# Optimization experiments

Hardware: AMD Instinct MI355X
Metric: run time of the kernel (lower is better)

Reference implementation:

```python
import jax, jax.numpy as jnp
import numpy as np

B, S, I, H = 32, 512, 1024, 1024


def _rnn_pass(x, W_ih, W_hh, b_ih, b_hh):
    # x: [B,S,I]; vanilla tanh RNN, h0 = 0. Precompute input projection once.
    xp = jnp.einsum('bsi,hi->bsh', x, W_ih) + b_ih + b_hh  # [B,S,H]
    h0 = jnp.zeros((x.shape[0], W_hh.shape[0]), dtype=x.dtype)

    def step(h, xp_t):
        h_new = jnp.tanh(xp_t + h @ W_hh.T)
        return h_new, h_new

    _, outs = jax.lax.scan(step, h0, jnp.swapaxes(xp, 0, 1))  # [S,B,H]
    return jnp.swapaxes(outs, 0, 1)  # [B,S,H]


def setup_inputs() -> dict:
    key = jax.random.key(0)
    ks = jax.random.split(key, 9)
    scale_i = 1.0 / np.sqrt(I)
    scale_h = 1.0 / np.sqrt(H)
    return {
        'x': jax.random.normal(ks[0], (B, S, I), dtype=jnp.float32),
        'W_ih_f': jax.random.normal(ks[1], (H, I), dtype=jnp.float32) * scale_i,
        'W_hh_f': jax.random.normal(ks[2], (H, H), dtype=jnp.float32) * scale_h,
        'b_ih_f': jax.random.normal(ks[3], (H,), dtype=jnp.float32) * scale_h,
        'b_hh_f': jax.random.normal(ks[4], (H,), dtype=jnp.float32) * scale_h,
        'W_ih_b': jax.random.normal(ks[5], (H, I), dtype=jnp.float32) * scale_i,
        'W_hh_b': jax.random.normal(ks[6], (H, H), dtype=jnp.float32) * scale_h,
        'b_ih_b': jax.random.normal(ks[7], (H,), dtype=jnp.float32) * scale_h,
        'b_hh_b': jax.random.normal(ks[8], (H,), dtype=jnp.float32) * scale_h,
    }


def reference(x, W_ih_f, W_hh_f, b_ih_f, b_hh_f, W_ih_b, W_hh_b, b_ih_b, b_hh_b):
    fwd = _rnn_pass(x, W_ih_f, W_hh_f, b_ih_f, b_hh_f)              # [B,S,H]
    bwd = _rnn_pass(x[:, ::-1, :], W_ih_b, W_hh_b, b_ih_b, b_hh_b)  # reversed seq
    bwd = bwd[:, ::-1, :]                                           # flip back
    return jnp.concatenate([fwd, bwd], axis=-1)  # [B,S,2H]
```

## Files before the change

kernel.cpp:

```cpp
#include <hip/hip_runtime.h>

typedef _Float16 half8  __attribute__((ext_vector_type(8)));
typedef _Float16 half4v __attribute__((ext_vector_type(4)));
typedef float    floatx4 __attribute__((ext_vector_type(4)));
typedef unsigned long long u64;

#define B_ 32
#define S_ 512
#define I_ 1024
#define H_ 1024
#define M_TOT (B_ * S_)

__global__ void cvt_f32_f16(const float* __restrict__ src, _Float16* __restrict__ dst, long n) {
  long i = ((long)blockIdx.x * blockDim.x + threadIdx.x) * 4;
  const long stride = (long)gridDim.x * blockDim.x * 4;
  for (; i < n; i += stride) {
    floatx4 v = *(const floatx4*)(src + i);
    half4v h = {(_Float16)v[0], (_Float16)v[1], (_Float16)v[2], (_Float16)v[3]};
    *(half4v*)(dst + i) = h;
  }
}

__global__ void bias_sum_kernel(const float* __restrict__ bihf, const float* __restrict__ bhhf,
                                const float* __restrict__ bihb, const float* __restrict__ bhhb,
                                float* __restrict__ bias, unsigned int* __restrict__ counter) {
  int i = blockIdx.x * blockDim.x + threadIdx.x;
  if (i == 0) {
    __hip_atomic_store(counter,      0u, __ATOMIC_RELAXED, __HIP_MEMORY_SCOPE_AGENT);
    __hip_atomic_store(counter + 32, 0u, __ATOMIC_RELAXED, __HIP_MEMORY_SCOPE_AGENT);
  }
  if (i < H_) {
    bias[i]      = bihf[i] + bhhf[i];
    bias[H_ + i] = bihb[i] + bhhb[i];
  }
}

__global__ void __launch_bounds__(256) gemm_xp_kernel(
    const _Float16* __restrict__ A,
    const _Float16* __restrict__ W,
    const float*    __restrict__ bias,
    float*          __restrict__ out)
{
  __shared__ _Float16 alds[128 * 32];
  __shared__ _Float16 blds[128 * 32];

  const int dir = blockIdx.z;
  const int m0  = blockIdx.y * 128;
  const int n0  = blockIdx.x * 128;
  const int tid  = threadIdx.x;
  const int lane = tid & 63;
  const int wv   = tid >> 6;
  const int wm   = wv >> 1, wn = wv & 1;
  const int lrow = lane & 15;
  const int lkg  = lane >> 4;

  const _Float16* Wd = W + (long)dir * H_ * I_;

  floatx4 acc[4][4] = {};

  const int srow = tid >> 1;
  const int sseg = tid & 1;

  for (int kt = 0; kt < 32; ++kt) {
    __syncthreads();
    {
      const _Float16* srcA = A  + (long)(m0 + srow) * I_ + kt * 32 + sseg * 16;
      const _Float16* srcB = Wd + (long)(n0 + srow) * I_ + kt * 32 + sseg * 16;
      half8 a0 = *(const half8*)(srcA);
      half8 a1 = *(const half8*)(srcA + 8);
      half8 b0 = *(const half8*)(srcB);
      half8 b1 = *(const half8*)(srcB + 8);
      const int sw = (srow & 7) << 4;
      const int base = srow * 64 + sseg * 32;
      *(half8*)((char*)alds + ((base     ) ^ sw)) = a0;
      *(half8*)((char*)alds + ((base + 16) ^ sw)) = a1;
      *(half8*)((char*)blds + ((base     ) ^ sw)) = b0;
      *(half8*)((char*)blds + ((base + 16) ^ sw)) = b1;
    }
    __syncthreads();

    half8 af[4], bf[4];
#pragma unroll
    for (int mt = 0; mt < 4; ++mt) {
      int r = wm * 64 + mt * 16 + lrow;
      int byte = (r * 64 + lkg * 16) ^ ((r & 7) << 4);
      af[mt] = *(const half8*)((const char*)alds + byte);
    }
#pragma unroll
    for (int ntt = 0; ntt < 4; ++ntt) {
      int r = wn * 64 + ntt * 16 + lrow;
      int byte = (r * 64 + lkg * 16) ^ ((r & 7) << 4);
      bf[ntt] = *(const half8*)((const char*)blds + byte);
    }
#pragma unroll
    for (int mt = 0; mt < 4; ++mt)
#pragma unroll
      for (int ntt = 0; ntt < 4; ++ntt)
        acc[mt][ntt] = __builtin_amdgcn_mfma_f32_16x16x32_f16(af[mt], bf[ntt], acc[mt][ntt], 0, 0, 0);
  }

#pragma unroll
  for (int mt = 0; mt < 4; ++mt) {
    int mrow = m0 + wm * 64 + mt * 16 + lkg * 4;
#pragma unroll
    for (int ntt = 0; ntt < 4; ++ntt) {
      int n = n0 + wn * 64 + ntt * 16 + lrow;
      float bv = bias[dir * H_ + n];
#pragma unroll
      for (int v = 0; v < 4; ++v) {
        out[(long)(mrow + v) * (2 * H_) + dir * H_ + n] = acc[mt][ntt][v] + bv;
      }
    }
  }
}

__global__ void __launch_bounds__(256, 1) scan_kernel(
    const float* __restrict__ Whh_f,
    const float* __restrict__ Whh_b,
    float*       __restrict__ out,
    _Float16*    __restrict__ hbuf,
    unsigned int* __restrict__ counter)
{
  __shared__ _Float16 wlds[32 * 1024];
  __shared__ floatx4  redlds[4 * 64];

  const int w     = blockIdx.x;
  const int dir   = w >> 5;
  const int rows0 = (w & 31) * 32;
  const float* Whh = dir ? Whh_b : Whh_f;
  unsigned int* ctr = counter + dir * 32;
  const int tid = threadIdx.x;

  for (int idx = tid; idx < 32 * 128; idx += 256) {
    const int r  = idx >> 7;
    const int kg = idx & 127;
    const float* src = Whh + (long)(rows0 + r) * H_ + kg * 8;
    floatx4 v0 = *(const floatx4*)(src);
    floatx4 v1 = *(const floatx4*)(src + 4);
    half8 h = {(_Float16)v0[0], (_Float16)v0[1], (_Float16)v0[2], (_Float16)v0[3],
               (_Float16)v1[0], (_Float16)v1[1], (_Float16)v1[2], (_Float16)v1[3]};
    const int byte = (r * 2048 + kg * 16) ^ ((r & 7) << 4);
    *(half8*)((char*)wlds + byte) = h;
  }

  {
    const int b  = tid >> 3;
    const int rg = tid & 7;
    u64* p = (u64*)(hbuf + ((long)(0 * 2 + dir) * B_ + b) * H_ + rows0 + rg * 4);
    __hip_atomic_store(p, (u64)0, __ATOMIC_RELAXED, __HIP_MEMORY_SCOPE_AGENT);
  }

  const int lane = tid & 63;
  const int wv   = tid >> 6;
  const int nt   = wv & 1;
  const int kh   = wv >> 1;
  const int lrow = lane & 15;
  const int lkg  = lane >> 4;
  const int b_idx = nt * 16 + lrow;
  const int kbase = kh * 512;
  const int r0    = rows0 + kh * 16 + lkg * 4;
  const int asw   = (lrow & 7) << 4;
  const int abase0 = lrow * 2048 + kbase * 2;
  const int abase1 = (16 + lrow) * 2048 + kbase * 2;

  unsigned int bar = 32;

  asm volatile("s_waitcnt vmcnt(0)" ::: "memory");
  __syncthreads();
  if (tid == 0) {
    __hip_atomic_fetch_add(ctr, 1u, __ATOMIC_RELAXED, __HIP_MEMORY_SCOPE_AGENT);
    while (__hip_atomic_load(ctr, __ATOMIC_RELAXED, __HIP_MEMORY_SCOPE_AGENT) < bar) {
      __builtin_amdgcn_s_sleep(1);
    }
  }
  __syncthreads();

  long o_next;
  {
    const int sidx = dir ? (S_ - 1) : 0;
    o_next = ((long)b_idx * S_ + sidx) * (2 * H_) + dir * H_ + r0;
  }
  floatx4 xp_next = *(const floatx4*)(out + o_next);

  for (int t = 0; t < S_; ++t) {
    const int p = t & 1;

    const _Float16* hp = hbuf + ((long)(p * 2 + dir) * B_ + b_idx) * H_ + kbase + lkg * 8;
    half8 hr[16];
#pragma unroll
    for (int kt = 0; kt < 16; ++kt) {
      asm volatile("global_load_dwordx4 %0, %1, off offset:%2 sc1"
                   : "=v"(hr[kt]) : "v"(hp), "i"(kt * 64) : "memory");
    }
    asm volatile("s_waitcnt vmcnt(0)" ::: "memory");
    __builtin_amdgcn_sched_barrier(0);

    floatx4 acc0 = {}, acc1 = {};
#pragma unroll
    for (int kt = 0; kt < 16; ++kt) {
      const int koff = kt * 64 + lkg * 16;
      half8 a0 = *(const half8*)((const char*)wlds + ((abase0 + koff) ^ asw));
      half8 a1 = *(const half8*)((const char*)wlds + ((abase1 + koff) ^ asw));
      acc0 = __builtin_amdgcn_mfma_f32_16x16x32_f16(a0, hr[kt], acc0, 0, 0, 0);
      acc1 = __builtin_amdgcn_mfma_f32_16x16x32_f16(a1, hr[kt], acc1, 0, 0, 0);
    }

    redlds[((1 - kh) * 2 + nt) * 64 + lane] = kh ? acc0 : acc1;
    __syncthreads();
    floatx4 tot = (kh ? acc1 : acc0) + redlds[(kh * 2 + nt) * 64 + lane];

    const long o = o_next;
    const floatx4 xpv = xp_next;
    if (t + 1 < S_) {
      const int sidx1 = dir ? (S_ - 2 - t) : (t + 1);
      o_next = ((long)b_idx * S_ + sidx1) * (2 * H_) + dir * H_ + r0;
      xp_next = *(const floatx4*)(out + o_next);
    }

    floatx4 hv;
#pragma unroll
    for (int v = 0; v < 4; ++v) {
      float z = tot[v] + xpv[v];
      hv[v] = 1.f - 2.f / (__expf(2.f * z) + 1.f);
    }
    *(floatx4*)(out + o) = hv;

    if (t + 1 < S_) {
      union { half4v h; u64 u; } hh;
      hh.h = half4v{(_Float16)hv[0], (_Float16)hv[1], (_Float16)hv[2], (_Float16)hv[3]};
      u64* dst = (u64*)(hbuf + ((long)((1 - p) * 2 + dir) * B_ + b_idx) * H_ + r0);
      __hip_atomic_store(dst, hh.u, __ATOMIC_RELAXED, __HIP_MEMORY_SCOPE_AGENT);
    } else {
      break;
    }

    bar += 32;
    asm volatile("s_waitcnt vmcnt(0)" ::: "memory");
    __syncthreads();
    if (tid == 0) {
      __hip_atomic_fetch_add(ctr, 1u, __ATOMIC_RELAXED, __HIP_MEMORY_SCOPE_AGENT);
      while (__hip_atomic_load(ctr, __ATOMIC_RELAXED, __HIP_MEMORY_SCOPE_AGENT) < bar) {
        __builtin_amdgcn_s_sleep(1);
      }
    }
    __syncthreads();
  }
}

extern "C" void kernel_launch(void* const* d_in, const int* in_sizes, int n_in,
                              void* d_out, int out_size, void* d_ws, size_t ws_size,
                              hipStream_t stream) {
  const float* x    = (const float*)d_in[0];
  const float* Wihf = (const float*)d_in[1];
  const float* Whhf = (const float*)d_in[2];
  const float* bihf = (const float*)d_in[3];
  const float* bhhf = (const float*)d_in[4];
  const float* Wihb = (const float*)d_in[5];
  const float* Whhb = (const float*)d_in[6];
  const float* bihb = (const float*)d_in[7];
  const float* bhhb = (const float*)d_in[8];
  float* out = (float*)d_out;

  char* ws = (char*)d_ws;
  _Float16*     x16  = (_Float16*)ws;
  _Float16*     w16  = (_Float16*)(ws + 33554432u);
  float*        bias = (float*)   (ws + 33554432u + 4194304u);
  _Float16*     hbuf = (_Float16*)(ws + 37756928u);
  unsigned int* counter = (unsigned int*)(ws + 38019072u);

  cvt_f32_f16<<<4096, 256, 0, stream>>>(x, x16, (long)M_TOT * I_);
  cvt_f32_f16<<<1024, 256, 0, stream>>>(Wihf, w16, (long)H_ * I_);
  cvt_f32_f16<<<1024, 256, 0, stream>>>(Wihb, w16 + (long)H_ * I_, (long)H_ * I_);
  bias_sum_kernel<<<4, 256, 0, stream>>>(bihf, bhhf, bihb, bhhb, bias, counter);

  dim3 g(H_ / 128, M_TOT / 128, 2);
  gemm_xp_kernel<<<g, 256, 0, stream>>>(x16, w16, bias, out);

  void* args[] = {(void*)&Whhf, (void*)&Whhb, (void*)&out, (void*)&hbuf, (void*)&counter};
  (void)hipLaunchCooperativeKernel((void*)scan_kernel, dim3(64), dim3(256),
                                   args, 0, stream);
}
```

Before: 2.446 ms.

## Interleave forward and backward RNN steps per block with split barrier counters

Each of the 64 blocks now owns 16 hidden rows of both directions rather than 32 rows of one direction, and it alternates forward and backward step computation. Each direction gets its own arrival counter. A block signals one direction, then computes the other direction before waiting on the first, so the latency of the grid-wide barrier is meant to overlap with useful MFMA work. In exchange, each block does two smaller matvecs per step with more __syncthreads. The per-step work per block also becomes more serialized, and the extra global counter traffic adds risk.

```diff
diff --git a/kernel.cpp b/kernel.cpp
--- a/kernel.cpp
+++ b/kernel.cpp
@@ -28,6 +28,7 @@
   if (i == 0) {
     __hip_atomic_store(counter,      0u, __ATOMIC_RELAXED, __HIP_MEMORY_SCOPE_AGENT);
     __hip_atomic_store(counter + 32, 0u, __ATOMIC_RELAXED, __HIP_MEMORY_SCOPE_AGENT);
+    __hip_atomic_store(counter + 64, 0u, __ATOMIC_RELAXED, __HIP_MEMORY_SCOPE_AGENT);
   }
   if (i < H_) {
     bias[i]      = bihf[i] + bhhf[i];
@@ -121,34 +122,45 @@
     _Float16*    __restrict__ hbuf,
     unsigned int* __restrict__ counter)
 {
-  __shared__ _Float16 wlds[32 * 1024];
-  __shared__ floatx4  redlds[4 * 64];
-
-  const int w     = blockIdx.x;
-  const int dir   = w >> 5;
-  const int rows0 = (w & 31) * 32;
-  const float* Whh = dir ? Whh_b : Whh_f;
-  unsigned int* ctr = counter + dir * 32;
-  const int tid = threadIdx.x;
-
-  for (int idx = tid; idx < 32 * 128; idx += 256) {
-    const int r  = idx >> 7;
+  __shared__ _Float16 wlds[2 * 16 * 1024];
+  __shared__ floatx4  redlds[128];
+
+  const int rb    = blockIdx.x;
+  const int rows0 = rb * 16;
+  const int tid   = threadIdx.x;
+  unsigned int* ctr_f = counter + 32;
+  unsigned int* ctr_b = counter + 64;
+
+  for (int idx = tid; idx < 2 * 16 * 128; idx += 256) {
+    const int d  = idx >> 11;
+    const int r  = (idx >> 7) & 15;
     const int kg = idx & 127;
-    const float* src = Whh + (long)(rows0 + r) * H_ + kg * 8;
+    const float* W = d ? Whh_b : Whh_f;
+    const float* src = W + (long)(rows0 + r) * H_ + kg * 8;
     floatx4 v0 = *(const floatx4*)(src);
     floatx4 v1 = *(const floatx4*)(src + 4);
     half8 h = {(_Float16)v0[0], (_Float16)v0[1], (_Float16)v0[2], (_Float16)v0[3],
                (_Float16)v1[0], (_Float16)v1[1], (_Float16)v1[2], (_Float16)v1[3]};
-    const int byte = (r * 2048 + kg * 16) ^ ((r & 7) << 4);
+    const int byte = d * 32768 + ((r * 2048 + kg * 16) ^ ((r & 7) << 4));
     *(half8*)((char*)wlds + byte) = h;
   }
 
   {
-    const int b  = tid >> 3;
-    const int rg = tid & 7;
-    u64* p = (u64*)(hbuf + ((long)(0 * 2 + dir) * B_ + b) * H_ + rows0 + rg * 4);
+    const int d  = tid >> 7;
+    const int b  = (tid >> 2) & 31;
+    const int rg = tid & 3;
+    u64* p = (u64*)(hbuf + ((long)(0 * 2 + d) * B_ + b) * H_ + rows0 + rg * 4);
     __hip_atomic_store(p, (u64)0, __ATOMIC_RELAXED, __HIP_MEMORY_SCOPE_AGENT);
   }
+
+  asm volatile("s_waitcnt vmcnt(0)" ::: "memory");
+  __syncthreads();
+  if (tid == 0) {
+    __hip_atomic_fetch_add(counter, 1u, __ATOMIC_RELAXED, __HIP_MEMORY_SCOPE_AGENT);
+    while (__hip_atomic_load(counter, __ATOMIC_RELAXED, __HIP_MEMORY_SCOPE_AGENT) < 64u)
+      __builtin_amdgcn_s_sleep(1);
+  }
+  __syncthreads();
 
   const int lane = tid & 63;
   const int wv   = tid >> 6;
@@ -158,92 +170,144 @@
   const int lkg  = lane >> 4;
   const int b_idx = nt * 16 + lrow;
   const int kbase = kh * 512;
-  const int r0    = rows0 + kh * 16 + lkg * 4;
+  const int r0    = rows0 + lkg * 4;
   const int asw   = (lrow & 7) << 4;
-  const int abase0 = lrow * 2048 + kbase * 2;
-  const int abase1 = (16 + lrow) * 2048 + kbase * 2;
-
-  unsigned int bar = 32;
-
-  asm volatile("s_waitcnt vmcnt(0)" ::: "memory");
-  __syncthreads();
-  if (tid == 0) {
-    __hip_atomic_fetch_add(ctr, 1u, __ATOMIC_RELAXED, __HIP_MEMORY_SCOPE_AGENT);
-    while (__hip_atomic_load(ctr, __ATOMIC_RELAXED, __HIP_MEMORY_SCOPE_AGENT) < bar) {
-      __builtin_amdgcn_s_sleep(1);
-    }
-  }
-  __syncthreads();
-
-  long o_next;
-  {
-    const int sidx = dir ? (S_ - 1) : 0;
-    o_next = ((long)b_idx * S_ + sidx) * (2 * H_) + dir * H_ + r0;
-  }
-  floatx4 xp_next = *(const floatx4*)(out + o_next);
-
+  const int abase_f = lrow * 2048 + kbase * 2;
+  const int abase_b = 32768 + lrow * 2048 + kbase * 2;
+
+  long o_f = 0, o_b = 0;
+  floatx4 xp_f = {}, xp_b = {};
+  if (kh == 0) {
+    o_f = ((long)b_idx * S_ + 0) * (2 * H_) + 0 * H_ + r0;
+    o_b = ((long)b_idx * S_ + (S_ - 1)) * (2 * H_) + 1 * H_ + r0;
+    xp_f = *(const floatx4*)(out + o_f);
+    xp_b = *(const floatx4*)(out + o_b);
+  }
+
+#pragma unroll 1
   for (int t = 0; t < S_; ++t) {
+    const bool last = (t == S_ - 1);
     const int p = t & 1;
 
-    const _Float16* hp = hbuf + ((long)(p * 2 + dir) * B_ + b_idx) * H_ + kbase + lkg * 8;
-    half8 hr[16];
-#pragma unroll
-    for (int kt = 0; kt < 16; ++kt) {
-      asm volatile("global_load_dwordx4 %0, %1, off offset:%2 sc1"
-                   : "=v"(hr[kt]) : "v"(hp), "i"(kt * 64) : "memory");
-    }
-    asm volatile("s_waitcnt vmcnt(0)" ::: "memory");
-    __builtin_amdgcn_sched_barrier(0);
-
-    floatx4 acc0 = {}, acc1 = {};
-#pragma unroll
-    for (int kt = 0; kt < 16; ++kt) {
-      const int koff = kt * 64 + lkg * 16;
-      half8 a0 = *(const half8*)((const char*)wlds + ((abase0 + koff) ^ asw));
-      half8 a1 = *(const half8*)((const char*)wlds + ((abase1 + koff) ^ asw));
-      acc0 = __builtin_amdgcn_mfma_f32_16x16x32_f16(a0, hr[kt], acc0, 0, 0, 0);
-      acc1 = __builtin_amdgcn_mfma_f32_16x16x32_f16(a1, hr[kt], acc1, 0, 0, 0);
-    }
-
-    redlds[((1 - kh) * 2 + nt) * 64 + lane] = kh ? acc0 : acc1;
-    __syncthreads();
-    floatx4 tot = (kh ? acc1 : acc0) + redlds[(kh * 2 + nt) * 64 + lane];
-
-    const long o = o_next;
-    const floatx4 xpv = xp_next;
-    if (t + 1 < S_) {
-      const int sidx1 = dir ? (S_ - 2 - t) : (t + 1);
-      o_next = ((long)b_idx * S_ + sidx1) * (2 * H_) + dir * H_ + r0;
-      xp_next = *(const floatx4*)(out + o_next);
-    }
-
-    floatx4 hv;
-#pragma unroll
-    for (int v = 0; v < 4; ++v) {
-      float z = tot[v] + xpv[v];
-      hv[v] = 1.f - 2.f / (__expf(2.f * z) + 1.f);
-    }
-    *(floatx4*)(out + o) = hv;
-
-    if (t + 1 < S_) {
-      union { half4v h; u64 u; } hh;
-      hh.h = half4v{(_Float16)hv[0], (_Float16)hv[1], (_Float16)hv[2], (_Float16)hv[3]};
-      u64* dst = (u64*)(hbuf + ((long)((1 - p) * 2 + dir) * B_ + b_idx) * H_ + r0);
-      __hip_atomic_store(dst, hh.u, __ATOMIC_RELAXED, __HIP_MEMORY_SCOPE_AGENT);
-    } else {
-      break;
-    }
-
-    bar += 32;
-    asm volatile("s_waitcnt vmcnt(0)" ::: "memory");
-    __syncthreads();
-    if (tid == 0) {
-      __hip_atomic_fetch_add(ctr, 1u, __ATOMIC_RELAXED, __HIP_MEMORY_SCOPE_AGENT);
-      while (__hip_atomic_load(ctr, __ATOMIC_RELAXED, __HIP_MEMORY_SCOPE_AGENT) < bar) {
-        __builtin_amdgcn_s_sleep(1);
-      }
-    }
-    __syncthreads();
+    {
+      const _Float16* hp = hbuf + ((long)(p * 2 + 0) * B_ + b_idx) * H_ + kbase + lkg * 8;
+      half8 hr[16];
+#pragma unroll
+      for (int kt = 0; kt < 16; ++kt)
+        asm volatile("global_load_dwordx4 %0, %1, off offset:%2 sc1"
+                     : "=v"(hr[kt]) : "v"(hp), "i"(kt * 64) : "memory");
+      asm volatile("s_waitcnt vmcnt(0)" ::: "memory");
+      __builtin_amdgcn_sched_barrier(0);
+
+      floatx4 a0 = {}, a1 = {};
+#pragma unroll
+      for (int kt = 0; kt < 16; ++kt) {
+        const int byte = (abase_f + kt * 64 + lkg * 16) ^ asw;
+        half8 a = *(const half8*)((const char*)wlds + byte);
+        if (kt & 1) a1 = __builtin_amdgcn_mfma_f32_16x16x32_f16(a, hr[kt], a1, 0, 0, 0);
+        else        a0 = __builtin_amdgcn_mfma_f32_16x16x32_f16(a, hr[kt], a0, 0, 0, 0);
+      }
+      floatx4 accs = a0 + a1;
+      if (kh == 1) redlds[nt * 64 + lane] = accs;
+      __syncthreads();
+
+      if (tid == 255) {
+        const unsigned int tgt = 64u * (unsigned)t;
+        unsigned int v = __hip_atomic_load(ctr_b, __ATOMIC_RELAXED, __HIP_MEMORY_SCOPE_AGENT);
+        while (v < tgt) {
+          __builtin_amdgcn_s_sleep(1);
+          v = __hip_atomic_load(ctr_b, __ATOMIC_RELAXED, __HIP_MEMORY_SCOPE_AGENT);
+        }
+      }
+
+      if (kh == 0) {
+        floatx4 tot = accs + redlds[nt * 64 + lane];
+        floatx4 hv;
+#pragma unroll
+        for (int v = 0; v < 4; ++v) {
+          float z = tot[v] + xp_f[v];
+          hv[v] = 1.f - 2.f / (__expf(2.f * z) + 1.f);
+        }
+        *(floatx4*)(out + o_f) = hv;
+        if (!last) {
+          union { half4v h; u64 u; } hh;
+          hh.h = half4v{(_Float16)hv[0], (_Float16)hv[1], (_Float16)hv[2], (_Float16)hv[3]};
+          u64* dst = (u64*)(hbuf + ((long)((1 - p) * 2 + 0) * B_ + b_idx) * H_ + r0);
+          __hip_atomic_store(dst, hh.u, __ATOMIC_RELAXED, __HIP_MEMORY_SCOPE_AGENT);
+        }
+      }
+
+      asm volatile("s_waitcnt vmcnt(0)" ::: "memory");
+      __syncthreads();
+      if (!last) {
+        if (tid == 0)
+          __hip_atomic_fetch_add(ctr_f, 1u, __ATOMIC_RELAXED, __HIP_MEMORY_SCOPE_AGENT);
+        if (kh == 0) {
+          o_f = ((long)b_idx * S_ + (t + 1)) * (2 * H_) + 0 * H_ + r0;
+          xp_f = *(const floatx4*)(out + o_f);
+        }
+      }
+    }
+
+    {
+      const _Float16* hp = hbuf + ((long)(p * 2 + 1) * B_ + b_idx) * H_ + kbase + lkg * 8;
+      half8 hr[16];
+#pragma unroll
+      for (int kt = 0; kt < 16; ++kt)
+        asm volatile("global_load_dwordx4 %0, %1, off offset:%2 sc1"
+                     : "=v"(hr[kt]) : "v"(hp), "i"(kt * 64) : "memory");
+      asm volatile("s_waitcnt vmcnt(0)" ::: "memory");
+      __builtin_amdgcn_sched_barrier(0);
+
+      floatx4 a0 = {}, a1 = {};
+#pragma unroll
+      for (int kt = 0; kt < 16; ++kt) {
+        const int byte = (abase_b + kt * 64 + lkg * 16) ^ asw;
+        half8 a = *(const half8*)((const char*)wlds + byte);
+        if (kt & 1) a1 = __builtin_amdgcn_mfma_f32_16x16x32_f16(a, hr[kt], a1, 0, 0, 0);
+        else        a0 = __builtin_amdgcn_mfma_f32_16x16x32_f16(a, hr[kt], a0, 0, 0, 0);
+      }
+      floatx4 accs = a0 + a1;
+      if (kh == 1) redlds[nt * 64 + lane] = accs;
+      __syncthreads();
+
+      if (tid == 255 && !last) {
+        const unsigned int tgt = 64u * (unsigned)(t + 1);
+        unsigned int v = __hip_atomic_load(ctr_f, __ATOMIC_RELAXED, __HIP_MEMORY_SCOPE_AGENT);
+        while (v < tgt) {
+          __builtin_amdgcn_s_sleep(1);
+          v = __hip_atomic_load(ctr_f, __ATOMIC_RELAXED, __HIP_MEMORY_SCOPE_AGENT);
+        }
+      }
+
+      if (kh == 0) {
+        floatx4 tot = accs + redlds[nt * 64 + lane];
+        floatx4 hv;
+#pragma unroll
+        for (int v = 0; v < 4; ++v) {
+          float z = tot[v] + xp_b[v];
+          hv[v] = 1.f - 2.f / (__expf(2.f * z) + 1.f);
+        }
+        *(floatx4*)(out + o_b) = hv;
+        if (!last) {
+          union { half4v h; u64 u; } hh;
+          hh.h = half4v{(_Float16)hv[0], (_Float16)hv[1], (_Float16)hv[2], (_Float16)hv[3]};
+          u64* dst = (u64*)(hbuf + ((long)((1 - p) * 2 + 1) * B_ + b_idx) * H_ + r0);
+          __hip_atomic_store(dst, hh.u, __ATOMIC_RELAXED, __HIP_MEMORY_SCOPE_AGENT);
+        }
+      }
+
+      asm volatile("s_waitcnt vmcnt(0)" ::: "memory");
+      __syncthreads();
+      if (!last) {
+        if (tid == 0)
+          __hip_atomic_fetch_add(ctr_b, 1u, __ATOMIC_RELAXED, __HIP_MEMORY_SCOPE_AGENT);
+        if (kh == 0) {
+          o_b = ((long)b_idx * S_ + (S_ - 2 - t)) * (2 * H_) + 1 * H_ + r0;
+          xp_b = *(const floatx4*)(out + o_b);
+        }
+      }
+    }
   }
 }
 
```

Result: slower. 3.412 ms (+39.5%).

## Replace per-step grid barrier with per-wave flag dataflow synchronization in RNN scan

Applied to the files above, without the earlier changes.

Drops the per-direction atomic counter barrier, which needed two __syncthreads and a fetch_add plus spin per step. Each wave now publishes a per-wave step flag after storing its slice of the hidden state. Before loading, each wave polls only the 32 flags of the producer waves covering its k-range. The reduction LDS buffer is double-buffered so the trailing block barrier can go away, letting waves run ahead independently. This cuts synchronization latency on the serial critical path, at the cost of more polling traffic and subtler memory-ordering assumptions under relaxed atomics.

```diff
diff --git a/kernel.cpp b/kernel.cpp
--- a/kernel.cpp
+++ b/kernel.cpp
@@ -23,11 +23,10 @@
 
 __global__ void bias_sum_kernel(const float* __restrict__ bihf, const float* __restrict__ bhhf,
                                 const float* __restrict__ bihb, const float* __restrict__ bhhb,
-                                float* __restrict__ bias, unsigned int* __restrict__ counter) {
+                                float* __restrict__ bias, unsigned int* __restrict__ flags) {
   int i = blockIdx.x * blockDim.x + threadIdx.x;
-  if (i == 0) {
-    __hip_atomic_store(counter,      0u, __ATOMIC_RELAXED, __HIP_MEMORY_SCOPE_AGENT);
-    __hip_atomic_store(counter + 32, 0u, __ATOMIC_RELAXED, __HIP_MEMORY_SCOPE_AGENT);
+  if (i < 256) {
+    __hip_atomic_store(flags + i, 0u, __ATOMIC_RELAXED, __HIP_MEMORY_SCOPE_AGENT);
   }
   if (i < H_) {
     bias[i]      = bihf[i] + bhhf[i];
@@ -119,16 +118,17 @@
     const float* __restrict__ Whh_b,
     float*       __restrict__ out,
     _Float16*    __restrict__ hbuf,
-    unsigned int* __restrict__ counter)
+    unsigned int* __restrict__ flags)
 {
   __shared__ _Float16 wlds[32 * 1024];
-  __shared__ floatx4  redlds[4 * 64];
+  __shared__ floatx4  redlds[2 * 4 * 64];
 
   const int w     = blockIdx.x;
   const int dir   = w >> 5;
-  const int rows0 = (w & 31) * 32;
+  const int rb    = w & 31;
+  const int rows0 = rb * 32;
   const float* Whh = dir ? Whh_b : Whh_f;
-  unsigned int* ctr = counter + dir * 32;
+  unsigned int* fl = flags + dir * 128;
   const int tid = threadIdx.x;
 
   for (int idx = tid; idx < 32 * 128; idx += 256) {
@@ -141,13 +141,6 @@
                (_Float16)v1[0], (_Float16)v1[1], (_Float16)v1[2], (_Float16)v1[3]};
     const int byte = (r * 2048 + kg * 16) ^ ((r & 7) << 4);
     *(half8*)((char*)wlds + byte) = h;
-  }
-
-  {
-    const int b  = tid >> 3;
-    const int rg = tid & 7;
-    u64* p = (u64*)(hbuf + ((long)(0 * 2 + dir) * B_ + b) * H_ + rows0 + rg * 4);
-    __hip_atomic_store(p, (u64)0, __ATOMIC_RELAXED, __HIP_MEMORY_SCOPE_AGENT);
   }
 
   const int lane = tid & 63;
@@ -163,60 +156,58 @@
   const int abase0 = lrow * 2048 + kbase * 2;
   const int abase1 = (16 + lrow) * 2048 + kbase * 2;
 
-  unsigned int bar = 32;
-
+  {
+    u64* pz = (u64*)(hbuf + ((long)(0 * 2 + dir) * B_ + b_idx) * H_ + r0);
+    __hip_atomic_store(pz, (u64)0, __ATOMIC_RELAXED, __HIP_MEMORY_SCOPE_AGENT);
+  }
   asm volatile("s_waitcnt vmcnt(0)" ::: "memory");
+  if (lane == 0)
+    __hip_atomic_store(&fl[rb * 4 + kh * 2 + nt], 1u, __ATOMIC_RELAXED, __HIP_MEMORY_SCOPE_AGENT);
   __syncthreads();
-  if (tid == 0) {
-    __hip_atomic_fetch_add(ctr, 1u, __ATOMIC_RELAXED, __HIP_MEMORY_SCOPE_AGENT);
-    while (__hip_atomic_load(ctr, __ATOMIC_RELAXED, __HIP_MEMORY_SCOPE_AGENT) < bar) {
-      __builtin_amdgcn_s_sleep(1);
-    }
-  }
-  __syncthreads();
-
-  long o_next;
-  {
-    const int sidx = dir ? (S_ - 1) : 0;
-    o_next = ((long)b_idx * S_ + sidx) * (2 * H_) + dir * H_ + r0;
-  }
-  floatx4 xp_next = *(const floatx4*)(out + o_next);
-
+
+  const int pl = lane & 31;
+  const unsigned int* fpoll = fl + (kh * 16 + (pl >> 1)) * 4 + (pl & 1) * 2 + nt;
+
+  long o_nxt = ((long)b_idx * S_ + (dir ? (S_ - 1) : 0)) * (2 * H_) + dir * H_ + r0;
+  floatx4 xp_n = *(const floatx4*)(out + o_nxt);
+
+#pragma unroll 1
   for (int t = 0; t < S_; ++t) {
     const int p = t & 1;
 
+    {
+      const unsigned int tgt = (unsigned)(t + 1);
+      while (true) {
+        unsigned int v = __hip_atomic_load(fpoll, __ATOMIC_RELAXED, __HIP_MEMORY_SCOPE_AGENT);
+        if (__all((int)(v >= tgt))) break;
+      }
+    }
+
     const _Float16* hp = hbuf + ((long)(p * 2 + dir) * B_ + b_idx) * H_ + kbase + lkg * 8;
     half8 hr[16];
 #pragma unroll
-    for (int kt = 0; kt < 16; ++kt) {
+    for (int kt = 0; kt < 16; ++kt)
       asm volatile("global_load_dwordx4 %0, %1, off offset:%2 sc1"
                    : "=v"(hr[kt]) : "v"(hp), "i"(kt * 64) : "memory");
-    }
     asm volatile("s_waitcnt vmcnt(0)" ::: "memory");
     __builtin_amdgcn_sched_barrier(0);
 
-    floatx4 acc0 = {}, acc1 = {};
+    floatx4 a0 = {}, a1 = {};
 #pragma unroll
     for (int kt = 0; kt < 16; ++kt) {
       const int koff = kt * 64 + lkg * 16;
-      half8 a0 = *(const half8*)((const char*)wlds + ((abase0 + koff) ^ asw));
-      half8 a1 = *(const half8*)((const char*)wlds + ((abase1 + koff) ^ asw));
-      acc0 = __builtin_amdgcn_mfma_f32_16x16x32_f16(a0, hr[kt], acc0, 0, 0, 0);
-      acc1 = __builtin_amdgcn_mfma_f32_16x16x32_f16(a1, hr[kt], acc1, 0, 0, 0);
-    }
-
-    redlds[((1 - kh) * 2 + nt) * 64 + lane] = kh ? acc0 : acc1;
+      half8 wa = *(const half8*)((const char*)wlds + ((abase0 + koff) ^ asw));
+      half8 wb = *(const half8*)((const char*)wlds + ((abase1 + koff) ^ asw));
+      a0 = __builtin_amdgcn_mfma_f32_16x16x32_f16(wa, hr[kt], a0, 0, 0, 0);
+      a1 = __builtin_amdgcn_mfma_f32_16x16x32_f16(wb, hr[kt], a1, 0, 0, 0);
+    }
+
+    redlds[(p * 4 + (1 - kh) * 2 + nt) * 64 + lane] = kh ? a0 : a1;
     __syncthreads();
-    floatx4 tot = (kh ? acc1 : acc0) + redlds[(kh * 2 + nt) * 64 + lane];
-
-    const long o = o_next;
-    const floatx4 xpv = xp_next;
-    if (t + 1 < S_) {
-      const int sidx1 = dir ? (S_ - 2 - t) : (t + 1);
-      o_next = ((long)b_idx * S_ + sidx1) * (2 * H_) + dir * H_ + r0;
-      xp_next = *(const floatx4*)(out + o_next);
-    }
-
+    floatx4 tot = (kh ? a1 : a0) + redlds[(p * 4 + kh * 2 + nt) * 64 + lane];
+
+    const long o = o_nxt;
+    const floatx4 xpv = xp_n;
     floatx4 hv;
 #pragma unroll
     for (int v = 0; v < 4; ++v) {
@@ -230,20 +221,14 @@
       hh.h = half4v{(_Float16)hv[0], (_Float16)hv[1], (_Float16)hv[2], (_Float16)hv[3]};
       u64* dst = (u64*)(hbuf + ((long)((1 - p) * 2 + dir) * B_ + b_idx) * H_ + r0);
       __hip_atomic_store(dst, hh.u, __ATOMIC_RELAXED, __HIP_MEMORY_SCOPE_AGENT);
-    } else {
-      break;
-    }
-
-    bar += 32;
-    asm volatile("s_waitcnt vmcnt(0)" ::: "memory");
-    __syncthreads();
-    if (tid == 0) {
-      __hip_atomic_fetch_add(ctr, 1u, __ATOMIC_RELAXED, __HIP_MEMORY_SCOPE_AGENT);
-      while (__hip_atomic_load(ctr, __ATOMIC_RELAXED, __HIP_MEMORY_SCOPE_AGENT) < bar) {
-        __builtin_amdgcn_s_sleep(1);
-      }
-    }
-    __syncthreads();
+      asm volatile("s_waitcnt vmcnt(0)" ::: "memory");
+      if (lane == 0)
+        __hip_atomic_store(&fl[rb * 4 + kh * 2 + nt], (unsigned)(t + 2),
+                           __ATOMIC_RELAXED, __HIP_MEMORY_SCOPE_AGENT);
+      const int sidx1 = dir ? (S_ - 2 - t) : (t + 1);
+      o_nxt = ((long)b_idx * S_ + sidx1) * (2 * H_) + dir * H_ + r0;
+      xp_n = *(const floatx4*)(out + o_nxt);
+    }
   }
 }
 
@@ -262,21 +247,21 @@
   float* out = (float*)d_out;
 
   char* ws = (char*)d_ws;
-  _Float16*     x16  = (_Float16*)ws;
-  _Float16*     w16  = (_Float16*)(ws + 33554432u);
-  float*        bias = (float*)   (ws + 33554432u + 4194304u);
-  _Float16*     hbuf = (_Float16*)(ws + 37756928u);
-  unsigned int* counter = (unsigned int*)(ws + 38019072u);
+  _Float16*     x16   = (_Float16*)ws;
+  _Float16*     w16   = (_Float16*)(ws + 33554432u);
+  float*        bias  = (float*)   (ws + 33554432u + 4194304u);
+  _Float16*     hbuf  = (_Float16*)(ws + 37756928u);
+  unsigned int* flags = (unsigned int*)(ws + 38019072u);
 
   cvt_f32_f16<<<4096, 256, 0, stream>>>(x, x16, (long)M_TOT * I_);
   cvt_f32_f16<<<1024, 256, 0, stream>>>(Wihf, w16, (long)H_ * I_);
   cvt_f32_f16<<<1024, 256, 0, stream>>>(Wihb, w16 + (long)H_ * I_, (long)H_ * I_);
-  bias_sum_kernel<<<4, 256, 0, stream>>>(bihf, bhhf, bihb, bhhb, bias, counter);
+  bias_sum_kernel<<<4, 256, 0, stream>>>(bihf, bhhf, bihb, bhhb, bias, flags);
 
   dim3 g(H_ / 128, M_TOT / 128, 2);
   gemm_xp_kernel<<<g, 256, 0, stream>>>(x16, w16, bias, out);
 
-  void* args[] = {(void*)&Whhf, (void*)&Whhb, (void*)&out, (void*)&hbuf, (void*)&counter};
+  void* args[] = {(void*)&Whhf, (void*)&Whhb, (void*)&out, (void*)&hbuf, (void*)&flags};
   (void)hipLaunchCooperativeKernel((void*)scan_kernel, dim3(64), dim3(256),
                                    args, 0, stream);
 }
```

Measured after the change: 3.110 ms. +27.2%, slower.
